# Kernel tuning notes

Hardware: AMD Instinct MI355X
Metric: run time of the kernel (lower is better)

Reference implementation:

```python
import jax, jax.numpy as jnp
import numpy as np

SPARSITY = 0.9  # fraction of zeros in the weight matrix


def setup_inputs() -> dict:
    key = jax.random.key(0)
    k_x, k_w, k_m, k_b = jax.random.split(key, 4)
    in_features, out_features = 4096, 4096
    n_tokens = 8192
    x = jax.random.normal(k_x, (n_tokens, in_features), dtype=jnp.float32)
    weight = jax.random.normal(k_w, (out_features, in_features), dtype=jnp.float32)
    mask = jax.random.uniform(k_m, (out_features, in_features)) >= SPARSITY
    bias = jax.random.normal(k_b, (out_features,), dtype=jnp.float32)
    return {"x": x, "weight": weight, "mask": mask, "bias": bias}


def reference(x, weight, mask, bias):
    # SparseLinear.forward: batch_addmm(weight_sparse, x, bias) == x @ W^T + b
    # The sparse CSR/COO weight is represented here as (dense values * mask).
    w = jnp.where(mask, weight, jnp.zeros((), dtype=weight.dtype))
    return jnp.einsum('ni,oi->no', x, w) + bias
```

## Files before the change

### kernel.cpp

```cpp
#include <hip/hip_runtime.h>
#include <hip/hip_bf16.h>
#include <stdint.h>


#define MDIM 8192
#define NDIM 4096
#define KDIM 4096

typedef __bf16   bf16x8 __attribute__((ext_vector_type(8)));
typedef float    f32x4  __attribute__((ext_vector_type(4)));
typedef uint16_t u16x8  __attribute__((ext_vector_type(8)));

__device__ __forceinline__ uint16_t f32_to_bf16_rne(float f) {
  union { float f; uint32_t u; } v; v.f = f;
  uint32_t u = v.u;
  return (uint16_t)((u + 0x7fffu + ((u >> 16) & 1u)) >> 16);
}

__global__ void detect_mask_kernel(const uint32_t* __restrict__ mask,
                                   int* __restrict__ flag) {
  __shared__ int any_nonbool;
  if (threadIdx.x == 0) any_nonbool = 0;
  __syncthreads();
  int bad = 0;
  for (int i = threadIdx.x; i < 4096; i += 256) {
    uint32_t w = mask[i];
    bad |= (w > 1u) ? 1 : 0;
  }
  if (bad) any_nonbool = 1;
  __syncthreads();
  if (threadIdx.x == 0) *flag = any_nonbool;
}

__global__ void cvt_x_kernel(const float* __restrict__ x,
                             uint16_t* __restrict__ xh, int n8) {
  const int stride = gridDim.x * blockDim.x;
  for (int i = blockIdx.x * blockDim.x + threadIdx.x; i < n8; i += stride) {
    const float4* src = (const float4*)x + (size_t)i * 2;
    float4 a = src[0], b = src[1];
    u16x8 o;
    o[0] = f32_to_bf16_rne(a.x); o[1] = f32_to_bf16_rne(a.y);
    o[2] = f32_to_bf16_rne(a.z); o[3] = f32_to_bf16_rne(a.w);
    o[4] = f32_to_bf16_rne(b.x); o[5] = f32_to_bf16_rne(b.y);
    o[6] = f32_to_bf16_rne(b.z); o[7] = f32_to_bf16_rne(b.w);
    *((u16x8*)xh + i) = o;
  }
}

__global__ void cvt_w_kernel(const float* __restrict__ w,
                             const void* __restrict__ mask,
                             const int* __restrict__ flag,
                             uint16_t* __restrict__ wh, int n8) {
  const int stride = gridDim.x * blockDim.x;
  const int isU8 = *flag;
  for (int i = blockIdx.x * blockDim.x + threadIdx.x; i < n8; i += stride) {
    const float4* src = (const float4*)w + (size_t)i * 2;
    float4 a = src[0], b = src[1];
    float vals[8] = {a.x, a.y, a.z, a.w, b.x, b.y, b.z, b.w};
    int m[8];
    if (isU8) {
      uint64_t mb = *((const uint64_t*)mask + i);
#pragma unroll
      for (int j = 0; j < 8; ++j) m[j] = (int)((mb >> (8 * j)) & 0xffu);
    } else {
      const int4* mp = (const int4*)mask + (size_t)i * 2;
      int4 ma = mp[0], mb4 = mp[1];
      m[0] = ma.x; m[1] = ma.y; m[2] = ma.z; m[3] = ma.w;
      m[4] = mb4.x; m[5] = mb4.y; m[6] = mb4.z; m[7] = mb4.w;
    }
    u16x8 o;
#pragma unroll
    for (int j = 0; j < 8; ++j)
      o[j] = m[j] ? f32_to_bf16_rne(vals[j]) : (uint16_t)0;
    *((u16x8*)wh + i) = o;
  }
}


#define BARRIER() do { asm volatile("" ::: "memory");            \
                       __builtin_amdgcn_s_barrier();             \
                       asm volatile("" ::: "memory"); } while (0)
#define WAITV8()  asm volatile("s_waitcnt vmcnt(8)" ::: "memory")
#define WAITV0()  asm volatile("s_waitcnt vmcnt(0)" ::: "memory")

__global__ __launch_bounds__(512, 2) void gemm_bias_256(
    const uint16_t* __restrict__ A, const uint16_t* __restrict__ B,
    const float* __restrict__ bias, float* __restrict__ C) {
  constexpr int BM = 256, BN = 256, BK = 64;
  constexpr int NT  = KDIM / BK;
  constexpr int NBN = NDIM / BN;

  __shared__ __align__(16) uint8_t smem[2 * 65536];

  const int bid = blockIdx.x;
  const int cpx = gridDim.x >> 3;
  const int wg  = (bid & 7) * cpx + (bid >> 3);
  const int bm  = wg / NBN, bn = wg % NBN;

  const int tid  = threadIdx.x;
  const int wave = tid >> 6, lane = tid & 63;
  const int wm = wave >> 2, wn = wave & 3;
  const int fr = lane & 15, fq = lane >> 4;

  const int trow = tid >> 3;
  const int tcb  = (tid & 7) << 4;
  const int tcol = (tcb ^ ((trow & 7) << 4)) >> 1;
  const uint16_t* Ab = A + (size_t)bm * BM * KDIM;
  const uint16_t* Bb = B + (size_t)bn * BN * KDIM;
  const size_t aoff = (size_t)trow * KDIM + tcol;

  const int c0 = ((fq) ^ (fr & 7)) << 4;
  const int c1 = ((4 + fq) ^ (fr & 7)) << 4;

  f32x4 acc[8][4] = {};

#define STAGE(tile, bufbase) do {                                              \
    const uint16_t* sa = Ab + (size_t)(tile) * BK + aoff;                      \
    const uint16_t* sb = Bb + (size_t)(tile) * BK + aoff;                      \
    _Pragma("unroll")                                                          \
    for (int is = 0; is < 4; ++is) {                                           \
      __builtin_amdgcn_global_load_lds(                                        \
          (const __attribute__((address_space(1))) void*)(sa + (size_t)is * 64 * KDIM), \
          (__attribute__((address_space(3))) void*)(smem + (bufbase) + is * 8192 + wave * 1024), \
          16, 0, 0);                                                           \
      __builtin_amdgcn_global_load_lds(                                        \
          (const __attribute__((address_space(1))) void*)(sb + (size_t)is * 64 * KDIM), \
          (__attribute__((address_space(3))) void*)(smem + (bufbase) + 32768 + is * 8192 + wave * 1024), \
          16, 0, 0);                                                           \
    }                                                                          \
  } while (0)

#define COMPUTE(bufbase) do {                                                  \
    const uint8_t* bA = smem + (bufbase);                                      \
    const uint8_t* bB = smem + (bufbase) + 32768;                              \
    bf16x8 bfrag[4][2];                                                        \
    _Pragma("unroll")                                                          \
    for (int ni = 0; ni < 4; ++ni) {                                           \
      const int brow = wn * 64 + ni * 16 + fr;                                 \
      bfrag[ni][0] = *(const bf16x8*)(bB + brow * 128 + c0);                   \
      bfrag[ni][1] = *(const bf16x8*)(bB + brow * 128 + c1);                   \
    }                                                                          \
    _Pragma("unroll")                                                          \
    for (int mh = 0; mh < 2; ++mh) {                                           \
      bf16x8 afrag[4][2];                                                      \
      _Pragma("unroll")                                                        \
      for (int mi = 0; mi < 4; ++mi) {                                         \
        const int arow = wm * 128 + mh * 64 + mi * 16 + fr;                    \
        afrag[mi][0] = *(const bf16x8*)(bA + arow * 128 + c0);                 \
        afrag[mi][1] = *(const bf16x8*)(bA + arow * 128 + c1);                 \
      }                                                                        \
      __builtin_amdgcn_s_setprio(1);                                          \
      _Pragma("unroll")                                                        \
      for (int mi = 0; mi < 4; ++mi)                                           \
        _Pragma("unroll")                                                      \
        for (int ni = 0; ni < 4; ++ni) {                                       \
          acc[mh * 4 + mi][ni] = __builtin_amdgcn_mfma_f32_16x16x32_bf16(      \
              afrag[mi][0], bfrag[ni][0], acc[mh * 4 + mi][ni], 0, 0, 0);      \
          acc[mh * 4 + mi][ni] = __builtin_amdgcn_mfma_f32_16x16x32_bf16(      \
              afrag[mi][1], bfrag[ni][1], acc[mh * 4 + mi][ni], 0, 0, 0);      \
        }                                                                      \
      __builtin_amdgcn_s_setprio(0);                                          \
    }                                                                          \
  } while (0)

  STAGE(0, 0);
  STAGE(1, 65536);
  WAITV8();
  BARRIER();

  for (int t = 0; t < NT; ++t) {
    const uint32_t bo = (uint32_t)(t & 1) * 65536u;
    COMPUTE(bo);
    BARRIER();
    if (t + 2 < NT) {
      STAGE(t + 2, bo);
      WAITV8();
      BARRIER();
    } else if (t + 1 < NT) {
      WAITV0();
      BARRIER();
    }
  }

  const int rowg0 = bm * BM + wm * 128 + fq * 4;
  const int colg0 = bn * BN + wn * 64 + fr;
#pragma unroll
  for (int ni = 0; ni < 4; ++ni) {
    const int col = colg0 + ni * 16;
    const float bv = bias[col];
#pragma unroll
    for (int mi = 0; mi < 8; ++mi) {
#pragma unroll
      for (int j = 0; j < 4; ++j) {
        const int row = rowg0 + mi * 16 + j;
        C[(size_t)row * NDIM + col] = acc[mi][ni][j] + bv;
      }
    }
  }
#undef STAGE
#undef COMPUTE
}

extern "C" void kernel_launch(void* const* d_in, const int* in_sizes, int n_in,
                              void* d_out, int out_size, void* d_ws, size_t ws_size,
                              hipStream_t stream) {
  const float* x    = (const float*)d_in[0];
  const float* w    = (const float*)d_in[1];
  const void*  mk   = (const void*)d_in[2];
  const float* bias = (const float*)d_in[3];
  float* out        = (float*)d_out;

  const size_t need = (size_t)MDIM * KDIM * 2 + (size_t)NDIM * KDIM * 2;
  if (ws_size < need) return;

  uint16_t* xh = (uint16_t*)d_ws;
  uint16_t* wh = xh + (size_t)MDIM * KDIM;

  int* flag = (int*)d_out;
  detect_mask_kernel<<<1, 256, 0, stream>>>((const uint32_t*)mk, flag);

  const int nx8 = MDIM * KDIM / 8;
  const int nw8 = NDIM * KDIM / 8;
  cvt_x_kernel<<<2048, 256, 0, stream>>>(x, xh, nx8);
  cvt_w_kernel<<<2048, 256, 0, stream>>>(w, mk, flag, wh, nw8);

  const int grid = (MDIM / 256) * (NDIM / 256);
  gemm_bias_256<<<grid, 512, 0, stream>>>(xh, wh, bias, out);
}
```

Before: 591.2 us.

## Switch GEMM to 32x32x16 MFMA with k-sliced phased LDS pipeline

Replaces the 16x16x32 MFMA inner loop with 32x32x16 MFMA on 16-wide accumulators. The shared-memory layout becomes k-slice-major (16-element slices per phase), and the staging of the next tile is interleaved with compute in four phases per tile, each waiting on vmcnt and synchronizing at a barrier. The goal is to overlap global-to-LDS loads with MFMA work more finely and to cut LDS fragment reads per MFMA. In exchange there are four barriers per tile instead of roughly two, and the unswizzled LDS layout may cause bank conflicts.

```diff
diff --git a/kernel.cpp b/kernel.cpp
--- a/kernel.cpp
+++ b/kernel.cpp
@@ -8,7 +8,7 @@
 #define KDIM 4096
 
 typedef __bf16   bf16x8 __attribute__((ext_vector_type(8)));
-typedef float    f32x4  __attribute__((ext_vector_type(4)));
+typedef float    f32x16 __attribute__((ext_vector_type(16)));
 typedef uint16_t u16x8  __attribute__((ext_vector_type(8)));
 
 __device__ __forceinline__ uint16_t f32_to_bf16_rne(float f) {
@@ -80,125 +80,105 @@
 #define BARRIER() do { asm volatile("" ::: "memory");            \
                        __builtin_amdgcn_s_barrier();             \
                        asm volatile("" ::: "memory"); } while (0)
-#define WAITV8()  asm volatile("s_waitcnt vmcnt(8)" ::: "memory")
-#define WAITV0()  asm volatile("s_waitcnt vmcnt(0)" ::: "memory")
+#define WAITV(n)  asm volatile("s_waitcnt vmcnt(" #n ")" ::: "memory")
 
 __global__ __launch_bounds__(512, 2) void gemm_bias_256(
     const uint16_t* __restrict__ A, const uint16_t* __restrict__ B,
     const float* __restrict__ bias, float* __restrict__ C) {
-  constexpr int BM = 256, BN = 256, BK = 64;
-  constexpr int NT  = KDIM / BK;
-  constexpr int NBN = NDIM / BN;
+  constexpr int NT = KDIM / 64;
 
   __shared__ __align__(16) uint8_t smem[2 * 65536];
 
   const int bid = blockIdx.x;
   const int cpx = gridDim.x >> 3;
   const int wg  = (bid & 7) * cpx + (bid >> 3);
-  const int bm  = wg / NBN, bn = wg % NBN;
+  const int bm  = wg / 16, bn = wg % 16;
 
   const int tid  = threadIdx.x;
   const int wave = tid >> 6, lane = tid & 63;
   const int wm = wave >> 2, wn = wave & 3;
-  const int fr = lane & 15, fq = lane >> 4;
-
-  const int trow = tid >> 3;
-  const int tcb  = (tid & 7) << 4;
-  const int tcol = (tcb ^ ((trow & 7) << 4)) >> 1;
-  const uint16_t* Ab = A + (size_t)bm * BM * KDIM;
-  const uint16_t* Bb = B + (size_t)bn * BN * KDIM;
-  const size_t aoff = (size_t)trow * KDIM + tcol;
-
-  const int c0 = ((fq) ^ (fr & 7)) << 4;
-  const int c1 = ((4 + fq) ^ (fr & 7)) << 4;
-
-  f32x4 acc[8][4] = {};
-
-#define STAGE(tile, bufbase) do {                                              \
-    const uint16_t* sa = Ab + (size_t)(tile) * BK + aoff;                      \
-    const uint16_t* sb = Bb + (size_t)(tile) * BK + aoff;                      \
-    _Pragma("unroll")                                                          \
-    for (int is = 0; is < 4; ++is) {                                           \
-      __builtin_amdgcn_global_load_lds(                                        \
-          (const __attribute__((address_space(1))) void*)(sa + (size_t)is * 64 * KDIM), \
-          (__attribute__((address_space(3))) void*)(smem + (bufbase) + is * 8192 + wave * 1024), \
-          16, 0, 0);                                                           \
-      __builtin_amdgcn_global_load_lds(                                        \
-          (const __attribute__((address_space(1))) void*)(sb + (size_t)is * 64 * KDIM), \
-          (__attribute__((address_space(3))) void*)(smem + (bufbase) + 32768 + is * 8192 + wave * 1024), \
-          16, 0, 0);                                                           \
-    }                                                                          \
+  const int lr = lane & 31, lh = lane >> 5;
+
+  const size_t grow = (size_t)(tid & 255) * KDIM + (size_t)(tid >> 8) * 8;
+  const uint16_t* Ab = A + (size_t)bm * 256 * KDIM + grow;
+  const uint16_t* Bb = B + (size_t)bn * 256 * KDIM + grow;
+  const uint32_t sdst = (uint32_t)tid * 16;
+
+  const uint32_t aro = (uint32_t)(lh * 4096 + (wm * 128 + lr) * 16);
+  const uint32_t bro = (uint32_t)(8192 + lh * 4096 + (wn * 64 + lr) * 16);
+
+  f32x16 acc[4][2] = {};
+
+#define STAGE_SLICE(kelem, bufb, ph) do {                                      \
+    __builtin_amdgcn_global_load_lds(                                          \
+        (const __attribute__((address_space(1))) void*)(Ab + (kelem) + (ph) * 16), \
+        (__attribute__((address_space(3))) void*)(smem + (bufb) + (ph) * 16384 + sdst), \
+        16, 0, 0);                                                             \
+    __builtin_amdgcn_global_load_lds(                                          \
+        (const __attribute__((address_space(1))) void*)(Bb + (kelem) + (ph) * 16), \
+        (__attribute__((address_space(3))) void*)(smem + (bufb) + (ph) * 16384 + 8192 + sdst), \
+        16, 0, 0);                                                             \
   } while (0)
 
-#define COMPUTE(bufbase) do {                                                  \
-    const uint8_t* bA = smem + (bufbase);                                      \
-    const uint8_t* bB = smem + (bufbase) + 32768;                              \
-    bf16x8 bfrag[4][2];                                                        \
-    _Pragma("unroll")                                                          \
-    for (int ni = 0; ni < 4; ++ni) {                                           \
-      const int brow = wn * 64 + ni * 16 + fr;                                 \
-      bfrag[ni][0] = *(const bf16x8*)(bB + brow * 128 + c0);                   \
-      bfrag[ni][1] = *(const bf16x8*)(bB + brow * 128 + c1);                   \
-    }                                                                          \
-    _Pragma("unroll")                                                          \
-    for (int mh = 0; mh < 2; ++mh) {                                           \
-      bf16x8 afrag[4][2];                                                      \
-      _Pragma("unroll")                                                        \
-      for (int mi = 0; mi < 4; ++mi) {                                         \
-        const int arow = wm * 128 + mh * 64 + mi * 16 + fr;                    \
-        afrag[mi][0] = *(const bf16x8*)(bA + arow * 128 + c0);                 \
-        afrag[mi][1] = *(const bf16x8*)(bA + arow * 128 + c1);                 \
-      }                                                                        \
-      __builtin_amdgcn_s_setprio(1);                                          \
-      _Pragma("unroll")                                                        \
-      for (int mi = 0; mi < 4; ++mi)                                           \
-        _Pragma("unroll")                                                      \
-        for (int ni = 0; ni < 4; ++ni) {                                       \
-          acc[mh * 4 + mi][ni] = __builtin_amdgcn_mfma_f32_16x16x32_bf16(      \
-              afrag[mi][0], bfrag[ni][0], acc[mh * 4 + mi][ni], 0, 0, 0);      \
-          acc[mh * 4 + mi][ni] = __builtin_amdgcn_mfma_f32_16x16x32_bf16(      \
-              afrag[mi][1], bfrag[ni][1], acc[mh * 4 + mi][ni], 0, 0, 0);      \
-        }                                                                      \
-      __builtin_amdgcn_s_setprio(0);                                          \
-    }                                                                          \
+#define PHASE_COMPUTE(bufb, ph) do {                                           \
+    const uint8_t* sb_ = smem + (bufb) + (ph) * 16384;                         \
+    bf16x8 bf0 = *(const bf16x8*)(sb_ + bro);                                  \
+    bf16x8 bf1 = *(const bf16x8*)(sb_ + bro + 512);                            \
+    bf16x8 af0 = *(const bf16x8*)(sb_ + aro);                                  \
+    bf16x8 af1 = *(const bf16x8*)(sb_ + aro + 512);                            \
+    bf16x8 af2 = *(const bf16x8*)(sb_ + aro + 1024);                           \
+    bf16x8 af3 = *(const bf16x8*)(sb_ + aro + 1536);                           \
+    __builtin_amdgcn_s_setprio(1);                                             \
+    acc[0][0] = __builtin_amdgcn_mfma_f32_32x32x16_bf16(af0, bf0, acc[0][0], 0, 0, 0); \
+    acc[0][1] = __builtin_amdgcn_mfma_f32_32x32x16_bf16(af0, bf1, acc[0][1], 0, 0, 0); \
+    acc[1][0] = __builtin_amdgcn_mfma_f32_32x32x16_bf16(af1, bf0, acc[1][0], 0, 0, 0); \
+    acc[1][1] = __builtin_amdgcn_mfma_f32_32x32x16_bf16(af1, bf1, acc[1][1], 0, 0, 0); \
+    acc[2][0] = __builtin_amdgcn_mfma_f32_32x32x16_bf16(af2, bf0, acc[2][0], 0, 0, 0); \
+    acc[2][1] = __builtin_amdgcn_mfma_f32_32x32x16_bf16(af2, bf1, acc[2][1], 0, 0, 0); \
+    acc[3][0] = __builtin_amdgcn_mfma_f32_32x32x16_bf16(af3, bf0, acc[3][0], 0, 0, 0); \
+    acc[3][1] = __builtin_amdgcn_mfma_f32_32x32x16_bf16(af3, bf1, acc[3][1], 0, 0, 0); \
+    __builtin_amdgcn_s_setprio(0);                                             \
   } while (0)
 
-  STAGE(0, 0);
-  STAGE(1, 65536);
-  WAITV8();
-  BARRIER();
-
-  for (int t = 0; t < NT; ++t) {
-    const uint32_t bo = (uint32_t)(t & 1) * 65536u;
-    COMPUTE(bo);
-    BARRIER();
-    if (t + 2 < NT) {
-      STAGE(t + 2, bo);
-      WAITV8();
-      BARRIER();
-    } else if (t + 1 < NT) {
-      WAITV0();
-      BARRIER();
-    }
-  }
-
-  const int rowg0 = bm * BM + wm * 128 + fq * 4;
-  const int colg0 = bn * BN + wn * 64 + fr;
-#pragma unroll
-  for (int ni = 0; ni < 4; ++ni) {
-    const int col = colg0 + ni * 16;
+  STAGE_SLICE(0, 0, 0);
+  STAGE_SLICE(0, 0, 1);
+  STAGE_SLICE(0, 0, 2);
+  STAGE_SLICE(0, 0, 3);
+
+  for (int t = 0; t < NT - 1; ++t) {
+    const uint32_t bp = (uint32_t)(t & 1) * 65536u;
+    const uint32_t bq = bp ^ 65536u;
+    const int kn = (t + 1) * 64;
+    WAITV(6); BARRIER(); STAGE_SLICE(kn, bq, 0); PHASE_COMPUTE(bp, 0);
+    WAITV(6); BARRIER(); STAGE_SLICE(kn, bq, 1); PHASE_COMPUTE(bp, 1);
+    WAITV(6); BARRIER(); STAGE_SLICE(kn, bq, 2); PHASE_COMPUTE(bp, 2);
+    WAITV(6); BARRIER(); STAGE_SLICE(kn, bq, 3); PHASE_COMPUTE(bp, 3);
+  }
+  {
+    const uint32_t bp = (uint32_t)((NT - 1) & 1) * 65536u;
+    WAITV(6); BARRIER(); PHASE_COMPUTE(bp, 0);
+    WAITV(4); BARRIER(); PHASE_COMPUTE(bp, 1);
+    WAITV(2); BARRIER(); PHASE_COMPUTE(bp, 2);
+    WAITV(0); BARRIER(); PHASE_COMPUTE(bp, 3);
+  }
+
+  const int rowg = bm * 256 + wm * 128;
+  const int colg = bn * 256 + wn * 64 + lr;
+#pragma unroll
+  for (int ni = 0; ni < 2; ++ni) {
+    const int col = colg + ni * 32;
     const float bv = bias[col];
 #pragma unroll
-    for (int mi = 0; mi < 8; ++mi) {
-#pragma unroll
-      for (int j = 0; j < 4; ++j) {
-        const int row = rowg0 + mi * 16 + j;
-        C[(size_t)row * NDIM + col] = acc[mi][ni][j] + bv;
+    for (int mi = 0; mi < 4; ++mi) {
+#pragma unroll
+      for (int r = 0; r < 16; ++r) {
+        const int row = rowg + mi * 32 + (r & 3) + 8 * (r >> 2) + 4 * lh;
+        C[(size_t)row * NDIM + col] = acc[mi][ni][r] + bv;
       }
     }
   }
-#undef STAGE
-#undef COMPUTE
+#undef STAGE_SLICE
+#undef PHASE_COMPUTE
 }
 
 extern "C" void kernel_launch(void* const* d_in, const int* in_sizes, int n_in,
```

Result: slower. 853.8 us (+44.4%).
